# Performance work log

Measured on AMD Instinct MI355X. Metric: run time of the kernel, lower is better.

The kernel has to match this reference:

```python
import jax, jax.numpy as jnp
import numpy as np

EPS = 1e-5
HEADS = 16
HEAD_DIM = 64
SIG_SCALE = HEAD_DIM ** (-0.25)
DEFAULT_BIAS = -3.0

def layernorm(x, scale, offset):
    mu = jnp.mean(x, axis=-1, keepdims=True)
    var = jnp.mean(jnp.square(x - mu), axis=-1, keepdims=True)
    return (x - mu) * jax.lax.rsqrt(var + EPS) * scale + offset

def setup_inputs() -> dict:
    key = jax.random.key(0)
    ks = jax.random.split(key, 16)
    B, Nq, Nk, D, A = 2, 2048, 2048, 1024, 1024
    s = 0.02
    return {
        "query_feats": jax.random.normal(ks[0], (B, Nq, D), jnp.float32),
        "key_feats": jax.random.normal(ks[1], (B, Nk, D), jnp.float32),
        "Wq": jax.random.normal(ks[2], (A, D), jnp.float32) * s,
        "Wk": jax.random.normal(ks[3], (A, D), jnp.float32) * s,
        "Wv": jax.random.normal(ks[4], (A, D), jnp.float32) * s,
        "Wo": jax.random.normal(ks[5], (D, A), jnp.float32) * s,
        "qn_scale": jnp.ones((HEAD_DIM,), jnp.float32),
        "qn_bias": jnp.zeros((HEAD_DIM,), jnp.float32),
        "kn_scale": jnp.ones((HEAD_DIM,), jnp.float32),
        "kn_bias": jnp.zeros((HEAD_DIM,), jnp.float32),
        "ln_q_scale": jnp.ones((D,), jnp.float32),
        "ln_q_bias": jnp.zeros((D,), jnp.float32),
        "ln_out_scale": jnp.ones((D,), jnp.float32),
        "ln_out_bias": jnp.zeros((D,), jnp.float32),
        "gamma": jnp.full((D,), 1e-5, jnp.float32),
    }

def reference(query_feats, key_feats, Wq, Wk, Wv, Wo, qn_scale, qn_bias, kn_scale, kn_bias, ln_q_scale, ln_q_bias, ln_out_scale, ln_out_bias, gamma):
    B, Nq, _ = query_feats.shape
    Nk = key_feats.shape[1]
    residual = query_feats
    xq = layernorm(query_feats, ln_q_scale, ln_q_bias)  # norm_first
    # projections (torch Linear: x @ W.T)
    q = (xq @ Wq.T).reshape(B, Nq, HEADS, HEAD_DIM).transpose(0, 2, 1, 3)
    k = (key_feats @ Wk.T).reshape(B, Nk, HEADS, HEAD_DIM).transpose(0, 2, 1, 3)
    v = (key_feats @ Wv.T).reshape(B, Nk, HEADS, HEAD_DIM).transpose(0, 2, 1, 3)
    # qk-norm over head_dim, then fixed sigmoid scale
    q = layernorm(q, qn_scale, qn_bias) * SIG_SCALE
    k = layernorm(k, kn_scale, kn_bias) * SIG_SCALE
    scores = jnp.einsum('bhqd,bhkd->bhqk', q, k) + DEFAULT_BIAS
    # hardware-optimized sigmoid: 0.5*(1+tanh(0.5*x))
    attn = 0.5 * (1.0 + jnp.tanh(0.5 * scores))
    ctx = jnp.einsum('bhqk,bhkd->bhqd', attn, v)
    ctx = ctx.transpose(0, 2, 1, 3).reshape(B, Nq, HEADS * HEAD_DIM)
    out = ctx @ Wo.T
    out = gamma * out
    out = residual + out
    out = layernorm(out, ln_out_scale, ln_out_bias)  # post_norm
    return out
```

## Files before the change

### kernel.cpp

```cpp
#include <hip/hip_runtime.h>

typedef unsigned short u16;
typedef unsigned int u32;
typedef __bf16 bf16x8 __attribute__((ext_vector_type(8)));
typedef float f32x4 __attribute__((ext_vector_type(4)));
typedef float f32x16 __attribute__((ext_vector_type(16)));
typedef u16 u16x8 __attribute__((ext_vector_type(8)));
typedef u16 u16x4 __attribute__((ext_vector_type(4)));
typedef u32 u32x4 __attribute__((ext_vector_type(4)));

#define LN_EPS 1e-5f
#define SIG_SCALE_F 0.35355339059327379f
#define NLOG2E -1.4426950408889634f
#define BIAS_L2E 4.328085122666891f

__device__ __forceinline__ u16 f2bf(float f) {
    u32 u = __builtin_bit_cast(u32, f);
    u32 r = u + 0x7fffu + ((u >> 16) & 1u);
    return (u16)(r >> 16);
}
__device__ __forceinline__ float bf2f(u16 v) {
    return __builtin_bit_cast(float, (u32)v << 16);
}
__device__ __forceinline__ u32 pk_hi(float a, float b) {
    return __builtin_amdgcn_perm(__builtin_bit_cast(u32, b), __builtin_bit_cast(u32, a),
                                 0x07060302u);
}

__device__ __forceinline__ void gload16(const u16* g, u16* lds) {
    __builtin_amdgcn_global_load_lds(
        (const __attribute__((address_space(1))) u32*)g,
        (__attribute__((address_space(3))) u32*)lds, 16, 0, 0);
}

__device__ __forceinline__ void gemm_core(f32x4 acc[4][4],
                                          const u16* __restrict__ A, const u16* __restrict__ B,
                                          int Kiter, int lda, int ldb,
                                          long m0, long n0, u16* As, u16* Bs) {
    const int tid = threadIdx.x;
    const int lane = tid & 63;
    const int wave = tid >> 6;
    const int r15 = lane & 15;
    const int qd = lane >> 4;
    const int wm = (wave >> 1) * 64;
    const int wn = (wave & 1) * 64;

    const int srow = wave * 16 + (lane >> 2);
    const int c0 = (lane & 3) ^ (srow & 3);
    const u16* Ap0 = A + (m0 + srow) * lda + c0 * 8;
    const u16* Ap1 = A + (m0 + srow + 64) * lda + c0 * 8;
    const u16* Bp0 = B + (n0 + srow) * ldb + c0 * 8;
    const u16* Bp1 = B + (n0 + srow + 64) * ldb + c0 * 8;
    u16* As0 = As + wave * 512;
    u16* As1 = As + (wave + 4) * 512;
    u16* Bs0 = Bs + wave * 512;
    u16* Bs1 = Bs + (wave + 4) * 512;

    for (int kt = 0; kt < Kiter; kt += 32) {
        __syncthreads();
        gload16(Ap0 + kt, As0);
        gload16(Ap1 + kt, As1);
        gload16(Bp0 + kt, Bs0);
        gload16(Bp1 + kt, Bs1);
        __syncthreads();
        bf16x8 af[4], bfr[4];
#pragma unroll
        for (int i = 0; i < 4; i++) {
            int row = wm + i * 16 + r15;
            af[i] = *(const bf16x8*)(As + row * 32 + ((qd ^ (row & 3)) * 8));
        }
#pragma unroll
        for (int j = 0; j < 4; j++) {
            int row = wn + j * 16 + r15;
            bfr[j] = *(const bf16x8*)(Bs + row * 32 + ((qd ^ (row & 3)) * 8));
        }
#pragma unroll
        for (int i = 0; i < 4; i++)
#pragma unroll
            for (int j = 0; j < 4; j++)
                acc[i][j] = __builtin_amdgcn_mfma_f32_16x16x32_bf16(af[i], bfr[j], acc[i][j], 0, 0, 0);
    }
}

__global__ __launch_bounds__(256) void gemm_qkv(const u16* __restrict__ xq, const u16* __restrict__ keyb,
                                                const u16* __restrict__ Wqb, const u16* __restrict__ Wkb,
                                                const u16* __restrict__ Wvb,
                                                const float* __restrict__ qns, const float* __restrict__ qnb,
                                                const float* __restrict__ kns, const float* __restrict__ knb,
                                                u16* __restrict__ qln, u16* __restrict__ kln,
                                                u16* __restrict__ vb) {
    __shared__ __attribute__((aligned(16))) u16 As[128 * 32];
    __shared__ __attribute__((aligned(16))) u16 Bs[128 * 32];
    const int z = blockIdx.z;
    const u16* A = (z == 0) ? xq : keyb;
    const u16* B = (z == 0) ? Wqb : ((z == 1) ? Wkb : Wvb);
    u16* C = (z == 0) ? qln : ((z == 1) ? kln : vb);
    const long m0 = (long)blockIdx.x * 128;
    const long n0 = (long)blockIdx.y * 128;

    f32x4 acc[4][4];
#pragma unroll
    for (int i = 0; i < 4; i++)
#pragma unroll
        for (int j = 0; j < 4; j++) acc[i][j] = (f32x4){0.f, 0.f, 0.f, 0.f};

    gemm_core(acc, A, B, 1024, 1024, 1024, m0, n0, As, Bs);

    const int lane = threadIdx.x & 63;
    const int wave = threadIdx.x >> 6;
    const int r15 = lane & 15;
    const int qd = lane >> 4;
    const int wm = (wave >> 1) * 64;
    const int wn = (wave & 1) * 64;

    if (z <= 1) {
        const float* sc_ = (z == 0) ? qns : kns;
        const float* bs_ = (z == 0) ? qnb : knb;
        float scl[4], bia[4];
#pragma unroll
        for (int j = 0; j < 4; j++) {
            scl[j] = sc_[j * 16 + r15] * SIG_SCALE_F;
            bia[j] = bs_[j * 16 + r15] * SIG_SCALE_F;
        }
#pragma unroll
        for (int i = 0; i < 4; i++) {
#pragma unroll
            for (int rr = 0; rr < 4; rr++) {
                float a0 = acc[i][0][rr], a1 = acc[i][1][rr], a2 = acc[i][2][rr], a3 = acc[i][3][rr];
                float s1 = (a0 + a1) + (a2 + a3);
                float s2 = __builtin_fmaf(a3, a3,
                           __builtin_fmaf(a2, a2, __builtin_fmaf(a1, a1, a0 * a0)));
#pragma unroll
                for (int off = 1; off <= 8; off <<= 1) {
                    s1 += __shfl_xor(s1, off, 64);
                    s2 += __shfl_xor(s2, off, 64);
                }
                float mu = s1 * (1.0f / 64.0f);
                float var = __builtin_fmaf(-mu, mu, s2 * (1.0f / 64.0f));
                float rs = rsqrtf(var + LN_EPS);
                long row = m0 + wm + i * 16 + qd * 4 + rr;
#pragma unroll
                for (int j = 0; j < 4; j++) {
                    long col = n0 + wn + j * 16 + r15;
                    float o = __builtin_fmaf((acc[i][j][rr] - mu) * rs, scl[j], bia[j]);
                    C[row * 1024 + col] = f2bf(o);
                }
            }
        }
    } else {
#pragma unroll
        for (int i = 0; i < 4; i++)
#pragma unroll
            for (int rr = 0; rr < 4; rr++) {
                long row = m0 + wm + i * 16 + qd * 4 + rr;
#pragma unroll
                for (int j = 0; j < 4; j++)
                    C[row * 1024 + n0 + wn + j * 16 + r15] = f2bf(acc[i][j][rr]);
            }
    }
}

__global__ __launch_bounds__(256) void gemm_o(const u16* __restrict__ ctx, const u16* __restrict__ Wob,
                                              u16* __restrict__ opre0, u16* __restrict__ opre1) {
    __shared__ __attribute__((aligned(16))) u16 As[128 * 32];
    __shared__ __attribute__((aligned(16))) u16 Bs[128 * 32];
    const int z = blockIdx.z;
    const int koff = z * 512;
    u16* C = z ? opre1 : opre0;
    const long m0 = (long)blockIdx.x * 128;
    const long n0 = (long)blockIdx.y * 128;
    f32x4 acc[4][4];
#pragma unroll
    for (int i = 0; i < 4; i++)
#pragma unroll
        for (int j = 0; j < 4; j++) acc[i][j] = (f32x4){0.f, 0.f, 0.f, 0.f};
    gemm_core(acc, ctx + koff, Wob + koff, 512, 1024, 1024, m0, n0, As, Bs);

    const int lane = threadIdx.x & 63;
    const int wave = threadIdx.x >> 6;
    const int r15 = lane & 15;
    const int qd = lane >> 4;
    const int wm = (wave >> 1) * 64;
    const int wn = (wave & 1) * 64;
#pragma unroll
    for (int i = 0; i < 4; i++)
#pragma unroll
        for (int rr = 0; rr < 4; rr++) {
            long row = m0 + wm + i * 16 + qd * 4 + rr;
#pragma unroll
            for (int j = 0; j < 4; j++)
                C[row * 1024 + n0 + wn + j * 16 + r15] = f2bf(acc[i][j][rr]);
        }
}

__device__ __forceinline__ bf16x8 frag64(const u16* base, int row, int kidx) {
    return *(const bf16x8*)(base + row * 64 + ((kidx ^ (row & 7)) * 8));
}

__global__ __launch_bounds__(256, 4) void attn_sigmoid_v4(const u16* __restrict__ q,
                                                          const u16* __restrict__ k,
                                                          const u16* __restrict__ vt,
                                                          u16* __restrict__ ctx0,
                                                          u16* __restrict__ ctx1) {
    __shared__ __attribute__((aligned(16))) u16 Qs[128 * 64];
    __shared__ __attribute__((aligned(16))) u16 Ks[64 * 64];
    __shared__ __attribute__((aligned(16))) u16 Vs[64 * 64];
    const int tid = threadIdx.x;
    const int lane = tid & 63;
    const int wave = tid >> 6;
    const int l31 = lane & 31;
    const int h = lane >> 5;
    const int q0 = (blockIdx.x & 15) * 128;
    const int kh = blockIdx.x >> 4;
    const int hd = blockIdx.y;
    const int b = blockIdx.z;
    const int bh = b * 16 + hd;
    u16* ctx = kh ? ctx1 : ctx0;

    const int lr0 = lane >> 3;
    const int lc0 = lane & 7;
    {
#pragma unroll
        for (int i = 0; i < 4; i++) {
            int s = wave * 4 + i;
            int row = s * 8 + lr0;
            int c = lc0 ^ (row & 7);
            gload16(q + (size_t)(b * 2048 + q0 + row) * 1024 + hd * 64 + c * 8, Qs + s * 512);
        }
    }
    __syncthreads();
    bf16x8 qB[4];
#pragma unroll
    for (int dblk = 0; dblk < 4; dblk++)
        qB[dblk] = frag64(Qs, wave * 32 + l31, dblk * 2 + h);

    f32x16 accO[2];
#pragma unroll
    for (int dt = 0; dt < 2; dt++)
#pragma unroll
        for (int r = 0; r < 16; r++) accO[dt][r] = 0.f;

    const int kbeg = kh * 1024;
    for (int kc = kbeg; kc < kbeg + 1024; kc += 64) {
        __syncthreads();
#pragma unroll
        for (int i = 0; i < 2; i++) {
            int s = wave * 2 + i;
            int row = s * 8 + lr0;
            int c = lc0 ^ (row & 7);
            gload16(k + (size_t)(b * 2048 + kc + row) * 1024 + hd * 64 + c * 8, Ks + s * 512);
            gload16(vt + (size_t)(bh * 64 + row) * 2048 + kc + c * 8, Vs + s * 512);
        }
        __syncthreads();

        f32x16 accS[2];
#pragma unroll
        for (int mt = 0; mt < 2; mt++) {
#pragma unroll
            for (int r = 0; r < 16; r++) accS[mt][r] = 0.f;
#pragma unroll
            for (int dblk = 0; dblk < 4; dblk++) {
                bf16x8 aK = frag64(Ks, mt * 32 + l31, dblk * 2 + h);
                accS[mt] = __builtin_amdgcn_mfma_f32_32x32x16_bf16(aK, qB[dblk], accS[mt], 0, 0, 0);
            }
        }

        u32 pg[2][4][2];
#pragma unroll
        for (int mt = 0; mt < 2; mt++)
#pragma unroll
            for (int g = 0; g < 4; g++) {
                float p[4];
#pragma unroll
                for (int e = 0; e < 4; e++) {
                    float t = __builtin_fmaf(accS[mt][g * 4 + e], NLOG2E, BIAS_L2E);
                    float u = __builtin_amdgcn_exp2f(t);
                    p[e] = __builtin_amdgcn_rcpf(1.0f + u);
                }
                pg[mt][g][0] = pk_hi(p[0], p[1]);
                pg[mt][g][1] = pk_hi(p[2], p[3]);
            }

#pragma unroll
        for (int mt = 0; mt < 2; mt++)
#pragma unroll
            for (int kblk = 0; kblk < 2; kblk++) {
                int glo = kblk * 2, ghi = kblk * 2 + 1;
                u32 x0 = (u32)__shfl_xor((int)pg[mt][glo][0], 32, 64);
                u32 x1 = (u32)__shfl_xor((int)pg[mt][glo][1], 32, 64);
                u32 y0 = (u32)__shfl_xor((int)pg[mt][ghi][0], 32, 64);
                u32 y1 = (u32)__shfl_xor((int)pg[mt][ghi][1], 32, 64);
                u32x4 fr;
                fr[0] = h ? y0 : pg[mt][glo][0];
                fr[1] = h ? y1 : pg[mt][glo][1];
                fr[2] = h ? pg[mt][ghi][0] : x0;
                fr[3] = h ? pg[mt][ghi][1] : x1;
                bf16x8 aP = __builtin_bit_cast(bf16x8, fr);
#pragma unroll
                for (int dt = 0; dt < 2; dt++) {
                    bf16x8 bV = frag64(Vs, dt * 32 + l31, mt * 4 + kblk * 2 + h);
                    accO[dt] = __builtin_amdgcn_mfma_f32_32x32x16_bf16(aP, bV, accO[dt], 0, 0, 0);
                }
            }
    }

#pragma unroll
    for (int dt = 0; dt < 2; dt++)
#pragma unroll
        for (int r = 0; r < 16; r++) {
            int qrow = q0 + wave * 32 + (r & 3) + 8 * (r >> 2) + 4 * h;
            ctx[(size_t)(b * 2048 + qrow) * 1024 + hd * 64 + dt * 32 + l31] = f2bf(accO[dt][r]);
        }
}

__global__ __launch_bounds__(256) void ctx_merge(const u16* __restrict__ a, const u16* __restrict__ b,
                                                 u16* __restrict__ c) {
    size_t i = ((size_t)blockIdx.x * 256 + threadIdx.x) * 8;
    u16x8 av = *(const u16x8*)(a + i);
    u16x8 bv = *(const u16x8*)(b + i);
    u16x8 o;
#pragma unroll
    for (int e = 0; e < 8; e++) o[e] = f2bf(bf2f(av[e]) + bf2f(bv[e]));
    *(u16x8*)(c + i) = o;
}

__global__ __launch_bounds__(256) void transpose_v(const u16* __restrict__ vb, u16* __restrict__ vt) {
    __shared__ u16 T[64 * 72];
    const int kt = blockIdx.x;
    const int bh = blockIdx.y;
    const int b = bh >> 4, h = bh & 15;
    const int tid = threadIdx.x;
    const int sr = tid >> 2, sc = (tid & 3) * 16;
    const u16* src = vb + (size_t)(b * 2048 + kt * 64 + sr) * 1024 + h * 64 + sc;
    *(u16x8*)&T[sr * 72 + sc] = *(const u16x8*)src;
    *(u16x8*)&T[sr * 72 + sc + 8] = *(const u16x8*)(src + 8);
    __syncthreads();
    u16x8 o0, o1;
#pragma unroll
    for (int i = 0; i < 8; i++) o0[i] = T[(sc + i) * 72 + sr];
#pragma unroll
    for (int i = 0; i < 8; i++) o1[i] = T[(sc + 8 + i) * 72 + sr];
    u16* dst = vt + (size_t)(bh * 64 + sr) * 2048 + kt * 64 + sc;
    *(u16x8*)dst = o0;
    *(u16x8*)(dst + 8) = o1;
}

__global__ __launch_bounds__(256) void ln_rows_bf16(const float* __restrict__ x,
                                                    const float* __restrict__ sc,
                                                    const float* __restrict__ bs,
                                                    u16* __restrict__ y) {
    __shared__ float s1buf[4], s2buf[4];
    const int row = blockIdx.x;
    const int tid = threadIdx.x;
    const size_t base = (size_t)row * 1024 + tid * 4;
    const float4 xv = *(const float4*)(x + base);
    float s1 = xv.x + xv.y + xv.z + xv.w;
    float s2 = xv.x * xv.x + xv.y * xv.y + xv.z * xv.z + xv.w * xv.w;
    int lane = tid & 63, wave = tid >> 6;
#pragma unroll
    for (int off = 32; off > 0; off >>= 1) {
        s1 += __shfl_down(s1, off, 64);
        s2 += __shfl_down(s2, off, 64);
    }
    if (lane == 0) { s1buf[wave] = s1; s2buf[wave] = s2; }
    __syncthreads();
    s1 = s1buf[0] + s1buf[1] + s1buf[2] + s1buf[3];
    s2 = s2buf[0] + s2buf[1] + s2buf[2] + s2buf[3];
    float mu = s1 * (1.0f / 1024.0f);
    float var = s2 * (1.0f / 1024.0f) - mu * mu;
    float rs = rsqrtf(var + LN_EPS);
    const float4 scv = *(const float4*)(sc + tid * 4);
    const float4 bsv = *(const float4*)(bs + tid * 4);
    u16x4 o;
    o[0] = f2bf((xv.x - mu) * rs * scv.x + bsv.x);
    o[1] = f2bf((xv.y - mu) * rs * scv.y + bsv.y);
    o[2] = f2bf((xv.z - mu) * rs * scv.z + bsv.z);
    o[3] = f2bf((xv.w - mu) * rs * scv.w + bsv.w);
    *(u16x4*)(y + base) = o;
}

__global__ __launch_bounds__(256) void final_ln(const float* __restrict__ resid,
                                                const u16* __restrict__ o0,
                                                const u16* __restrict__ o1,
                                                const float* __restrict__ gamma,
                                                const float* __restrict__ sc,
                                                const float* __restrict__ bs,
                                                float* __restrict__ out) {
    __shared__ float s1buf[4], s2buf[4];
    const int row = blockIdx.x;
    const int tid = threadIdx.x;
    const size_t base = (size_t)row * 1024 + tid * 4;
    float4 rv = *(const float4*)(resid + base);
    u16x4 p0 = *(const u16x4*)(o0 + base);
    u16x4 p1 = *(const u16x4*)(o1 + base);
    float4 gv = *(const float4*)(gamma + tid * 4);
    float4 xv;
    xv.x = rv.x + gv.x * (bf2f(p0[0]) + bf2f(p1[0]));
    xv.y = rv.y + gv.y * (bf2f(p0[1]) + bf2f(p1[1]));
    xv.z = rv.z + gv.z * (bf2f(p0[2]) + bf2f(p1[2]));
    xv.w = rv.w + gv.w * (bf2f(p0[3]) + bf2f(p1[3]));
    float s1 = xv.x + xv.y + xv.z + xv.w;
    float s2 = xv.x * xv.x + xv.y * xv.y + xv.z * xv.z + xv.w * xv.w;
    int lane = tid & 63, wave = tid >> 6;
#pragma unroll
    for (int off = 32; off > 0; off >>= 1) {
        s1 += __shfl_down(s1, off, 64);
        s2 += __shfl_down(s2, off, 64);
    }
    if (lane == 0) { s1buf[wave] = s1; s2buf[wave] = s2; }
    __syncthreads();
    s1 = s1buf[0] + s1buf[1] + s1buf[2] + s1buf[3];
    s2 = s2buf[0] + s2buf[1] + s2buf[2] + s2buf[3];
    float mu = s1 * (1.0f / 1024.0f);
    float var = s2 * (1.0f / 1024.0f) - mu * mu;
    float rs = rsqrtf(var + LN_EPS);
    const float4 scv = *(const float4*)(sc + tid * 4);
    const float4 bsv = *(const float4*)(bs + tid * 4);
    float4 o;
    o.x = (xv.x - mu) * rs * scv.x + bsv.x;
    o.y = (xv.y - mu) * rs * scv.y + bsv.y;
    o.z = (xv.z - mu) * rs * scv.z + bsv.z;
    o.w = (xv.w - mu) * rs * scv.w + bsv.w;
    *(float4*)(out + base) = o;
}

__global__ __launch_bounds__(256) void conv_all(const float* __restrict__ w0, const float* __restrict__ w1,
                                                const float* __restrict__ w2, const float* __restrict__ w3,
                                                const float* __restrict__ kf,
                                                u16* __restrict__ wdst, u16* __restrict__ kdst) {
    size_t e = ((size_t)blockIdx.x * 256 + threadIdx.x) * 4;
    const float* src;
    u16* dst;
    if (e < 4194304) {
        int w = (int)(e >> 20);
        size_t off = e & 1048575;
        src = ((w == 0) ? w0 : (w == 1) ? w1 : (w == 2) ? w2 : w3) + off;
        dst = wdst + e;
    } else {
        size_t off = e - 4194304;
        src = kf + off;
        dst = kdst + off;
    }
    float4 xv = *(const float4*)src;
    u16x4 o;
    o[0] = f2bf(xv.x);
    o[1] = f2bf(xv.y);
    o[2] = f2bf(xv.z);
    o[3] = f2bf(xv.w);
    *(u16x4*)dst = o;
}

extern "C" void kernel_launch(void* const* d_in, const int* in_sizes, int n_in,
                              void* d_out, int out_size, void* d_ws, size_t ws_size,
                              hipStream_t stream) {
    const float* qf    = (const float*)d_in[0];
    const float* kf    = (const float*)d_in[1];
    const float* Wq    = (const float*)d_in[2];
    const float* Wk    = (const float*)d_in[3];
    const float* Wv    = (const float*)d_in[4];
    const float* Wo    = (const float*)d_in[5];
    const float* qn_s  = (const float*)d_in[6];
    const float* qn_b  = (const float*)d_in[7];
    const float* kn_s  = (const float*)d_in[8];
    const float* kn_b  = (const float*)d_in[9];
    const float* lnq_s = (const float*)d_in[10];
    const float* lnq_b = (const float*)d_in[11];
    const float* lno_s = (const float*)d_in[12];
    const float* lno_b = (const float*)d_in[13];
    const float* gamma = (const float*)d_in[14];
    float* out = (float*)d_out;

    char* ws = (char*)d_ws;
    const size_t MB = 1024 * 1024;
    u16* Wqb   = (u16*)(ws + 0 * MB);
    u16* Wkb   = (u16*)(ws + 2 * MB);
    u16* Wvb   = (u16*)(ws + 4 * MB);
    u16* Wob   = (u16*)(ws + 6 * MB);
    u16* xq    = (u16*)(ws + 8 * MB);
    u16* ctx   = (u16*)(ws + 8 * MB);
    u16* keyb  = (u16*)(ws + 16 * MB);
    u16* opre0 = (u16*)(ws + 16 * MB);
    u16* qln   = (u16*)(ws + 24 * MB);
    u16* opre1 = (u16*)(ws + 24 * MB);
    u16* kln   = (u16*)(ws + 32 * MB);
    u16* vb    = (u16*)(ws + 40 * MB);
    u16* ctx1  = (u16*)(ws + 40 * MB);
    u16* vt    = (u16*)(ws + 48 * MB);
    u16* ctx0  = (u16*)(ws + 56 * MB);

    conv_all<<<dim3(6144), 256, 0, stream>>>(Wq, Wk, Wv, Wo, kf, Wqb, keyb);
    ln_rows_bf16<<<dim3(4096), 256, 0, stream>>>(qf, lnq_s, lnq_b, xq);

    gemm_qkv<<<dim3(32, 8, 3), 256, 0, stream>>>(xq, keyb, Wqb, Wkb, Wvb,
                                                 qn_s, qn_b, kn_s, kn_b, qln, kln, vb);

    transpose_v<<<dim3(32, 32), 256, 0, stream>>>(vb, vt);

    attn_sigmoid_v4<<<dim3(32, 16, 2), 256, 0, stream>>>(qln, kln, vt, ctx0, ctx1);
    ctx_merge<<<dim3(2048), 256, 0, stream>>>(ctx0, ctx1, ctx);

    gemm_o<<<dim3(32, 8, 2), 256, 0, stream>>>(ctx, Wob, opre0, opre1);
    final_ln<<<dim3(4096), 256, 0, stream>>>(qf, opre0, opre1, gamma, lno_s, lno_b, out);
}
```

Baseline: 250.6 us.

## Fuse prep kernels, merge attention split-K in-block, widen output split-K

Merges the weight/key bf16 conversion and the query layernorm into one prep launch. The attention kernel now splits the key range across wave pairs inside a block (64 queries per block) and reduces the two partial contexts through shared memory, so the separate ctx_merge kernel and its extra global round trip go away. The output projection uses a 4-way K split instead of 2, and final_ln sums four bf16 partials. The trade-offs are fewer query rows per block, which means more K/V reloads per query, and more partial-output traffic in the final reduction.

```diff
diff --git a/kernel.cpp b/kernel.cpp
--- a/kernel.cpp
+++ b/kernel.cpp
@@ -161,12 +161,12 @@
 }
 
 __global__ __launch_bounds__(256) void gemm_o(const u16* __restrict__ ctx, const u16* __restrict__ Wob,
-                                              u16* __restrict__ opre0, u16* __restrict__ opre1) {
+                                              u16* __restrict__ opre) {
     __shared__ __attribute__((aligned(16))) u16 As[128 * 32];
     __shared__ __attribute__((aligned(16))) u16 Bs[128 * 32];
     const int z = blockIdx.z;
-    const int koff = z * 512;
-    u16* C = z ? opre1 : opre0;
+    const int koff = z * 256;
+    u16* C = opre + (size_t)z * 4194304;
     const long m0 = (long)blockIdx.x * 128;
     const long n0 = (long)blockIdx.y * 128;
     f32x4 acc[4][4];
@@ -174,7 +174,7 @@
     for (int i = 0; i < 4; i++)
 #pragma unroll
         for (int j = 0; j < 4; j++) acc[i][j] = (f32x4){0.f, 0.f, 0.f, 0.f};
-    gemm_core(acc, ctx + koff, Wob + koff, 512, 1024, 1024, m0, n0, As, Bs);
+    gemm_core(acc, ctx + koff, Wob + koff, 256, 1024, 1024, m0, n0, As, Bs);
 
     const int lane = threadIdx.x & 63;
     const int wave = threadIdx.x >> 6;
@@ -197,61 +197,65 @@
     return *(const bf16x8*)(base + row * 64 + ((kidx ^ (row & 7)) * 8));
 }
 
-__global__ __launch_bounds__(256, 4) void attn_sigmoid_v4(const u16* __restrict__ q,
+__global__ __launch_bounds__(256, 4) void attn_sigmoid_v5(const u16* __restrict__ q,
                                                           const u16* __restrict__ k,
                                                           const u16* __restrict__ vt,
-                                                          u16* __restrict__ ctx0,
-                                                          u16* __restrict__ ctx1) {
-    __shared__ __attribute__((aligned(16))) u16 Qs[128 * 64];
-    __shared__ __attribute__((aligned(16))) u16 Ks[64 * 64];
-    __shared__ __attribute__((aligned(16))) u16 Vs[64 * 64];
+                                                          u16* __restrict__ ctx) {
+    __shared__ __attribute__((aligned(16))) u16 Sh[4096 + 8192 + 8192];
+    u16* Qs = Sh;
+    u16* Ks = Sh + 4096;
+    u16* Vs = Sh + 4096 + 8192;
+    float* Obuf = (float*)(Sh + 4096);
+
     const int tid = threadIdx.x;
     const int lane = tid & 63;
     const int wave = tid >> 6;
     const int l31 = lane & 31;
     const int h = lane >> 5;
-    const int q0 = (blockIdx.x & 15) * 128;
-    const int kh = blockIdx.x >> 4;
+    const int qsub = wave & 1;
+    const int kh = wave >> 1;
+    const int q0 = blockIdx.x * 64;
     const int hd = blockIdx.y;
     const int b = blockIdx.z;
     const int bh = b * 16 + hd;
-    u16* ctx = kh ? ctx1 : ctx0;
 
     const int lr0 = lane >> 3;
     const int lc0 = lane & 7;
     {
-#pragma unroll
-        for (int i = 0; i < 4; i++) {
-            int s = wave * 4 + i;
-            int row = s * 8 + lr0;
-            int c = lc0 ^ (row & 7);
-            gload16(q + (size_t)(b * 2048 + q0 + row) * 1024 + hd * 64 + c * 8, Qs + s * 512);
-        }
-    }
-    __syncthreads();
-    bf16x8 qB[4];
-#pragma unroll
-    for (int dblk = 0; dblk < 4; dblk++)
-        qB[dblk] = frag64(Qs, wave * 32 + l31, dblk * 2 + h);
-
-    f32x16 accO[2];
-#pragma unroll
-    for (int dt = 0; dt < 2; dt++)
-#pragma unroll
-        for (int r = 0; r < 16; r++) accO[dt][r] = 0.f;
-
-    const int kbeg = kh * 1024;
-    for (int kc = kbeg; kc < kbeg + 1024; kc += 64) {
-        __syncthreads();
 #pragma unroll
         for (int i = 0; i < 2; i++) {
             int s = wave * 2 + i;
             int row = s * 8 + lr0;
             int c = lc0 ^ (row & 7);
-            gload16(k + (size_t)(b * 2048 + kc + row) * 1024 + hd * 64 + c * 8, Ks + s * 512);
-            gload16(vt + (size_t)(bh * 64 + row) * 2048 + kc + c * 8, Vs + s * 512);
-        }
+            gload16(q + (size_t)(b * 2048 + q0 + row) * 1024 + hd * 64 + c * 8, Qs + s * 512);
+        }
+    }
+    __syncthreads();
+    bf16x8 qB[4];
+#pragma unroll
+    for (int dblk = 0; dblk < 4; dblk++)
+        qB[dblk] = frag64(Qs, qsub * 32 + l31, dblk * 2 + h);
+
+    f32x16 accO[2];
+#pragma unroll
+    for (int dt = 0; dt < 2; dt++)
+#pragma unroll
+        for (int r = 0; r < 16; r++) accO[dt][r] = 0.f;
+
+    u16* Ksh = Ks + kh * 4096;
+    u16* Vsh = Vs + kh * 4096;
+    const int kbeg = kh * 1024;
+    for (int kc = kbeg; kc < kbeg + 1024; kc += 64) {
         __syncthreads();
+#pragma unroll
+        for (int i = 0; i < 4; i++) {
+            int s = qsub * 4 + i;
+            int row = s * 8 + lr0;
+            int c = lc0 ^ (row & 7);
+            gload16(k + (size_t)(b * 2048 + kc + row) * 1024 + hd * 64 + c * 8, Ksh + s * 512);
+            gload16(vt + (size_t)(bh * 64 + row) * 2048 + kc + c * 8, Vsh + s * 512);
+        }
+        __syncthreads();
 
         f32x16 accS[2];
 #pragma unroll
@@ -260,7 +264,7 @@
             for (int r = 0; r < 16; r++) accS[mt][r] = 0.f;
 #pragma unroll
             for (int dblk = 0; dblk < 4; dblk++) {
-                bf16x8 aK = frag64(Ks, mt * 32 + l31, dblk * 2 + h);
+                bf16x8 aK = frag64(Ksh, mt * 32 + l31, dblk * 2 + h);
                 accS[mt] = __builtin_amdgcn_mfma_f32_32x32x16_bf16(aK, qB[dblk], accS[mt], 0, 0, 0);
             }
         }
@@ -298,30 +302,33 @@
                 bf16x8 aP = __builtin_bit_cast(bf16x8, fr);
 #pragma unroll
                 for (int dt = 0; dt < 2; dt++) {
-                    bf16x8 bV = frag64(Vs, dt * 32 + l31, mt * 4 + kblk * 2 + h);
+                    bf16x8 bV = frag64(Vsh, dt * 32 + l31, mt * 4 + kblk * 2 + h);
                     accO[dt] = __builtin_amdgcn_mfma_f32_32x32x16_bf16(aP, bV, accO[dt], 0, 0, 0);
                 }
             }
     }
 
-#pragma unroll
-    for (int dt = 0; dt < 2; dt++)
-#pragma unroll
-        for (int r = 0; r < 16; r++) {
-            int qrow = q0 + wave * 32 + (r & 3) + 8 * (r >> 2) + 4 * h;
-            ctx[(size_t)(b * 2048 + qrow) * 1024 + hd * 64 + dt * 32 + l31] = f2bf(accO[dt][r]);
-        }
-}
-
-__global__ __launch_bounds__(256) void ctx_merge(const u16* __restrict__ a, const u16* __restrict__ b,
-                                                 u16* __restrict__ c) {
-    size_t i = ((size_t)blockIdx.x * 256 + threadIdx.x) * 8;
-    u16x8 av = *(const u16x8*)(a + i);
-    u16x8 bv = *(const u16x8*)(b + i);
-    u16x8 o;
-#pragma unroll
-    for (int e = 0; e < 8; e++) o[e] = f2bf(bf2f(av[e]) + bf2f(bv[e]));
-    *(u16x8*)(c + i) = o;
+    __syncthreads();
+    if (kh == 1) {
+#pragma unroll
+        for (int dt = 0; dt < 2; dt++)
+#pragma unroll
+            for (int r = 0; r < 16; r++) {
+                int ql = qsub * 32 + (r & 3) + 8 * (r >> 2) + 4 * h;
+                Obuf[ql * 64 + dt * 32 + l31] = accO[dt][r];
+            }
+    }
+    __syncthreads();
+    if (kh == 0) {
+#pragma unroll
+        for (int dt = 0; dt < 2; dt++)
+#pragma unroll
+            for (int r = 0; r < 16; r++) {
+                int ql = qsub * 32 + (r & 3) + 8 * (r >> 2) + 4 * h;
+                float s = accO[dt][r] + Obuf[ql * 64 + dt * 32 + l31];
+                ctx[(size_t)(b * 2048 + q0 + ql) * 1024 + hd * 64 + dt * 32 + l31] = f2bf(s);
+            }
+    }
 }
 
 __global__ __launch_bounds__(256) void transpose_v(const u16* __restrict__ vb, u16* __restrict__ vt) {
@@ -345,43 +352,66 @@
     *(u16x8*)(dst + 8) = o1;
 }
 
-__global__ __launch_bounds__(256) void ln_rows_bf16(const float* __restrict__ x,
-                                                    const float* __restrict__ sc,
-                                                    const float* __restrict__ bs,
-                                                    u16* __restrict__ y) {
-    __shared__ float s1buf[4], s2buf[4];
-    const int row = blockIdx.x;
+__global__ __launch_bounds__(256) void prep(const float* __restrict__ w0, const float* __restrict__ w1,
+                                            const float* __restrict__ w2, const float* __restrict__ w3,
+                                            const float* __restrict__ kf, const float* __restrict__ qf,
+                                            const float* __restrict__ lnq_s, const float* __restrict__ lnq_b,
+                                            u16* __restrict__ wdst, u16* __restrict__ kdst,
+                                            u16* __restrict__ xq) {
+    const int bx = blockIdx.x;
     const int tid = threadIdx.x;
-    const size_t base = (size_t)row * 1024 + tid * 4;
-    const float4 xv = *(const float4*)(x + base);
-    float s1 = xv.x + xv.y + xv.z + xv.w;
-    float s2 = xv.x * xv.x + xv.y * xv.y + xv.z * xv.z + xv.w * xv.w;
-    int lane = tid & 63, wave = tid >> 6;
-#pragma unroll
-    for (int off = 32; off > 0; off >>= 1) {
-        s1 += __shfl_down(s1, off, 64);
-        s2 += __shfl_down(s2, off, 64);
-    }
-    if (lane == 0) { s1buf[wave] = s1; s2buf[wave] = s2; }
-    __syncthreads();
-    s1 = s1buf[0] + s1buf[1] + s1buf[2] + s1buf[3];
-    s2 = s2buf[0] + s2buf[1] + s2buf[2] + s2buf[3];
-    float mu = s1 * (1.0f / 1024.0f);
-    float var = s2 * (1.0f / 1024.0f) - mu * mu;
-    float rs = rsqrtf(var + LN_EPS);
-    const float4 scv = *(const float4*)(sc + tid * 4);
-    const float4 bsv = *(const float4*)(bs + tid * 4);
-    u16x4 o;
-    o[0] = f2bf((xv.x - mu) * rs * scv.x + bsv.x);
-    o[1] = f2bf((xv.y - mu) * rs * scv.y + bsv.y);
-    o[2] = f2bf((xv.z - mu) * rs * scv.z + bsv.z);
-    o[3] = f2bf((xv.w - mu) * rs * scv.w + bsv.w);
-    *(u16x4*)(y + base) = o;
+    if (bx < 6144) {
+        size_t e = ((size_t)bx * 256 + tid) * 4;
+        const float* src;
+        u16* dst;
+        if (e < 4194304) {
+            src = ((e >> 20) == 0 ? w0 : (e >> 20) == 1 ? w1 : (e >> 20) == 2 ? w2 : w3) + (e & 1048575);
+            dst = wdst + e;
+        } else {
+            size_t off = e - 4194304;
+            src = kf + off;
+            dst = kdst + off;
+        }
+        float4 xv = *(const float4*)src;
+        u16x4 o;
+        o[0] = f2bf(xv.x);
+        o[1] = f2bf(xv.y);
+        o[2] = f2bf(xv.z);
+        o[3] = f2bf(xv.w);
+        *(u16x4*)dst = o;
+    } else {
+        __shared__ float s1buf[4], s2buf[4];
+        const int row = bx - 6144;
+        const size_t base = (size_t)row * 1024 + tid * 4;
+        const float4 xv = *(const float4*)(qf + base);
+        float s1 = xv.x + xv.y + xv.z + xv.w;
+        float s2 = xv.x * xv.x + xv.y * xv.y + xv.z * xv.z + xv.w * xv.w;
+        int lane = tid & 63, wave = tid >> 6;
+#pragma unroll
+        for (int off = 32; off > 0; off >>= 1) {
+            s1 += __shfl_down(s1, off, 64);
+            s2 += __shfl_down(s2, off, 64);
+        }
+        if (lane == 0) { s1buf[wave] = s1; s2buf[wave] = s2; }
+        __syncthreads();
+        s1 = s1buf[0] + s1buf[1] + s1buf[2] + s1buf[3];
+        s2 = s2buf[0] + s2buf[1] + s2buf[2] + s2buf[3];
+        float mu = s1 * (1.0f / 1024.0f);
+        float var = s2 * (1.0f / 1024.0f) - mu * mu;
+        float rs = rsqrtf(var + LN_EPS);
+        const float4 scv = *(const float4*)(lnq_s + tid * 4);
+        const float4 bsv = *(const float4*)(lnq_b + tid * 4);
+        u16x4 o;
+        o[0] = f2bf((xv.x - mu) * rs * scv.x + bsv.x);
+        o[1] = f2bf((xv.y - mu) * rs * scv.y + bsv.y);
+        o[2] = f2bf((xv.z - mu) * rs * scv.z + bsv.z);
+        o[3] = f2bf((xv.w - mu) * rs * scv.w + bsv.w);
+        *(u16x4*)(xq + base) = o;
+    }
 }
 
 __global__ __launch_bounds__(256) void final_ln(const float* __restrict__ resid,
-                                                const u16* __restrict__ o0,
-                                                const u16* __restrict__ o1,
+                                                const u16* __restrict__ opre,
                                                 const float* __restrict__ gamma,
                                                 const float* __restrict__ sc,
                                                 const float* __restrict__ bs,
@@ -391,14 +421,16 @@
     const int tid = threadIdx.x;
     const size_t base = (size_t)row * 1024 + tid * 4;
     float4 rv = *(const float4*)(resid + base);
-    u16x4 p0 = *(const u16x4*)(o0 + base);
-    u16x4 p1 = *(const u16x4*)(o1 + base);
+    u16x4 p0 = *(const u16x4*)(opre + base);
+    u16x4 p1 = *(const u16x4*)(opre + 4194304 + base);
+    u16x4 p2 = *(const u16x4*)(opre + 8388608 + base);
+    u16x4 p3 = *(const u16x4*)(opre + 12582912 + base);
     float4 gv = *(const float4*)(gamma + tid * 4);
     float4 xv;
-    xv.x = rv.x + gv.x * (bf2f(p0[0]) + bf2f(p1[0]));
-    xv.y = rv.y + gv.y * (bf2f(p0[1]) + bf2f(p1[1]));
-    xv.z = rv.z + gv.z * (bf2f(p0[2]) + bf2f(p1[2]));
-    xv.w = rv.w + gv.w * (bf2f(p0[3]) + bf2f(p1[3]));
+    xv.x = rv.x + gv.x * ((bf2f(p0[0]) + bf2f(p1[0])) + (bf2f(p2[0]) + bf2f(p3[0])));
+    xv.y = rv.y + gv.y * ((bf2f(p0[1]) + bf2f(p1[1])) + (bf2f(p2[1]) + bf2f(p3[1])));
+    xv.z = rv.z + gv.z * ((bf2f(p0[2]) + bf2f(p1[2])) + (bf2f(p2[2]) + bf2f(p3[2])));
+    xv.w = rv.w + gv.w * ((bf2f(p0[3]) + bf2f(p1[3])) + (bf2f(p2[3]) + bf2f(p3[3])));
     float s1 = xv.x + xv.y + xv.z + xv.w;
     float s2 = xv.x * xv.x + xv.y * xv.y + xv.z * xv.z + xv.w * xv.w;
     int lane = tid & 63, wave = tid >> 6;
@@ -422,32 +454,6 @@
     o.z = (xv.z - mu) * rs * scv.z + bsv.z;
     o.w = (xv.w - mu) * rs * scv.w + bsv.w;
     *(float4*)(out + base) = o;
-}
-
-__global__ __launch_bounds__(256) void conv_all(const float* __restrict__ w0, const float* __restrict__ w1,
-                                                const float* __restrict__ w2, const float* __restrict__ w3,
-                                                const float* __restrict__ kf,
-                                                u16* __restrict__ wdst, u16* __restrict__ kdst) {
-    size_t e = ((size_t)blockIdx.x * 256 + threadIdx.x) * 4;
-    const float* src;
-    u16* dst;
-    if (e < 4194304) {
-        int w = (int)(e >> 20);
-        size_t off = e & 1048575;
-        src = ((w == 0) ? w0 : (w == 1) ? w1 : (w == 2) ? w2 : w3) + off;
-        dst = wdst + e;
-    } else {
-        size_t off = e - 4194304;
-        src = kf + off;
-        dst = kdst + off;
-    }
-    float4 xv = *(const float4*)src;
-    u16x4 o;
-    o[0] = f2bf(xv.x);
-    o[1] = f2bf(xv.y);
-    o[2] = f2bf(xv.z);
-    o[3] = f2bf(xv.w);
-    *(u16x4*)dst = o;
 }
 
 extern "C" void kernel_launch(void* const* d_in, const int* in_sizes, int n_in,
@@ -479,26 +485,21 @@
     u16* xq    = (u16*)(ws + 8 * MB);
     u16* ctx   = (u16*)(ws + 8 * MB);
     u16* keyb  = (u16*)(ws + 16 * MB);
-    u16* opre0 = (u16*)(ws + 16 * MB);
     u16* qln   = (u16*)(ws + 24 * MB);
-    u16* opre1 = (u16*)(ws + 24 * MB);
     u16* kln   = (u16*)(ws + 32 * MB);
     u16* vb    = (u16*)(ws + 40 * MB);
-    u16* ctx1  = (u16*)(ws + 40 * MB);
     u16* vt    = (u16*)(ws + 48 * MB);
-    u16* ctx0  = (u16*)(ws + 56 * MB);
-
-    conv_all<<<dim3(6144), 256, 0, stream>>>(Wq, Wk, Wv, Wo, kf, Wqb, keyb);
-    ln_rows_bf16<<<dim3(4096), 256, 0, stream>>>(qf, lnq_s, lnq_b, xq);
+    u16* opre  = (u16*)(ws + 24 * MB);
+
+    prep<<<dim3(10240), 256, 0, stream>>>(Wq, Wk, Wv, Wo, kf, qf, lnq_s, lnq_b, Wqb, keyb, xq);
 
     gemm_qkv<<<dim3(32, 8, 3), 256, 0, stream>>>(xq, keyb, Wqb, Wkb, Wvb,
                                                  qn_s, qn_b, kn_s, kn_b, qln, kln, vb);
 
     transpose_v<<<dim3(32, 32), 256, 0, stream>>>(vb, vt);
 
-    attn_sigmoid_v4<<<dim3(32, 16, 2), 256, 0, stream>>>(qln, kln, vt, ctx0, ctx1);
-    ctx_merge<<<dim3(2048), 256, 0, stream>>>(ctx0, ctx1, ctx);
-
-    gemm_o<<<dim3(32, 8, 2), 256, 0, stream>>>(ctx, Wob, opre0, opre1);
-    final_ln<<<dim3(4096), 256, 0, stream>>>(qf, opre0, opre1, gamma, lno_s, lno_b, out);
-}
+    attn_sigmoid_v5<<<dim3(32, 16, 2), 256, 0, stream>>>(qln, kln, vt, ctx);
+
+    gemm_o<<<dim3(32, 8, 4), 256, 0, stream>>>(ctx, Wob, opre);
+    final_ln<<<dim3(4096), 256, 0, stream>>>(qf, opre, gamma, lno_s, lno_b, out);
+}
```

New measurement: 249.4 us. No clear change (-0.5%).
